# Optimization experiments

Hardware: AMD Instinct MI355X
Metric: run time of the kernel (lower is better)

Reference implementation:

```python
import jax, jax.numpy as jnp
import numpy as np

D_MODEL = 768
N_HEADS = 12
HEAD_DIM = D_MODEL // N_HEADS
D_FF = 4 * D_MODEL
EPS = 1e-5


def setup_inputs() -> dict:
    key = jax.random.key(0)
    ks = jax.random.split(key, 16)
    s = 0.02
    x = jax.random.normal(ks[0], (2, 2048, D_MODEL), dtype=jnp.float32)
    wq = jax.random.normal(ks[1], (D_MODEL, D_MODEL), dtype=jnp.float32) * s
    bq = jnp.zeros((D_MODEL,), jnp.float32)
    wk = jax.random.normal(ks[2], (D_MODEL, D_MODEL), dtype=jnp.float32) * s
    bk = jnp.zeros((D_MODEL,), jnp.float32)
    wv = jax.random.normal(ks[3], (D_MODEL, D_MODEL), dtype=jnp.float32) * s
    bv = jnp.zeros((D_MODEL,), jnp.float32)
    wo = jax.random.normal(ks[4], (D_MODEL, D_MODEL), dtype=jnp.float32) * s
    bo = jnp.zeros((D_MODEL,), jnp.float32)
    w1 = jax.random.normal(ks[5], (D_MODEL, D_FF), dtype=jnp.float32) * s
    b1 = jnp.zeros((D_FF,), jnp.float32)
    w2 = jax.random.normal(ks[6], (D_FF, D_MODEL), dtype=jnp.float32) * s
    b2 = jnp.zeros((D_MODEL,), jnp.float32)
    ln1_g = jnp.ones((D_MODEL,), jnp.float32)
    ln1_b = jnp.zeros((D_MODEL,), jnp.float32)
    ln2_g = jnp.ones((D_MODEL,), jnp.float32)
    ln2_b = jnp.zeros((D_MODEL,), jnp.float32)
    return dict(x=x, wq=wq, bq=bq, wk=wk, bk=bk, wv=wv, bv=bv, wo=wo, bo=bo,
                w1=w1, b1=b1, w2=w2, b2=b2,
                ln1_g=ln1_g, ln1_b=ln1_b, ln2_g=ln2_g, ln2_b=ln2_b)


def _layernorm(x, g, b):
    mu = jnp.mean(x, axis=-1, keepdims=True)
    var = jnp.mean(jnp.square(x - mu), axis=-1, keepdims=True)
    return (x - mu) * jax.lax.rsqrt(var + EPS) * g + b


def _attention(x, wq, bq, wk, bk, wv, bv, wo, bo):
    B, S, D = x.shape
    def split_heads(t):  # [B,S,D] -> [B,H,S,Hd]
        return t.reshape(B, S, N_HEADS, HEAD_DIM).transpose(0, 2, 1, 3)
    q = split_heads(x @ wq + bq)
    k = split_heads(x @ wk + bk)
    v = split_heads(x @ wv + bv)
    scores = jnp.einsum('bhqd,bhkd->bhqk', q, k) / np.sqrt(HEAD_DIM).astype(np.float32)
    causal = jnp.tril(jnp.ones((S, S), dtype=bool))
    scores = jnp.where(causal, scores, -jnp.inf)
    weights = jax.nn.softmax(scores, axis=-1)
    attn = jnp.einsum('bhqk,bhkd->bhqd', weights, v)
    attn = attn.transpose(0, 2, 1, 3).reshape(B, S, D)
    return attn @ wo + bo


def reference(x, wq, bq, wk, bk, wv, bv, wo, bo, w1, b1, w2, b2,
              ln1_g, ln1_b, ln2_g, ln2_b):
    x = x + _attention(_layernorm(x, ln1_g, ln1_b), wq, bq, wk, bk, wv, bv, wo, bo)
    h = _layernorm(x, ln2_g, ln2_b)
    ff = jax.nn.relu(h @ w1 + b1) @ w2 + b2
    return x + ff
```

## Files before the change

kernel.cpp:

```cpp
#include <hip/hip_runtime.h>
#include <stdint.h>

typedef __bf16 bf16;
typedef float f32x4 __attribute__((ext_vector_type(4)));
typedef bf16 bf16x8 __attribute__((ext_vector_type(8)));
typedef bf16 bf16x4 __attribute__((ext_vector_type(4)));

#define MFMA16(a, b, c) __builtin_amdgcn_mfma_f32_16x16x32_bf16((a), (b), (c), 0, 0, 0)

static __device__ __forceinline__ void load_lds16(const bf16* g, bf16* l) {
  __builtin_amdgcn_global_load_lds(
      (const __attribute__((address_space(1))) void*)g,
      (__attribute__((address_space(3))) void*)l, 16, 0, 0);
}

__global__ void __launch_bounds__(256) k_transpose(
    const float* s0, const float* s1, const float* s2, const float* s3,
    const float* s4, const float* s5,
    bf16* d0, bf16* d1, bf16* d2, bf16* d3, bf16* d4, bf16* d5) {
  int z = blockIdx.z;
  const float* src; bf16* dst; int R, C;
  switch (z) {
    case 0: src = s0; dst = d0; R = 768;  C = 768;  break;
    case 1: src = s1; dst = d1; R = 768;  C = 768;  break;
    case 2: src = s2; dst = d2; R = 768;  C = 768;  break;
    case 3: src = s3; dst = d3; R = 768;  C = 768;  break;
    case 4: src = s4; dst = d4; R = 768;  C = 3072; break;
    default: src = s5; dst = d5; R = 3072; C = 768; break;
  }
  int tcn = C >> 5;
  int nt = (R >> 5) * tcn;
  int t = blockIdx.x;
  if (t >= nt) return;
  int tr = t / tcn, tc = t % tcn;
  __shared__ float tile[32][33];
  int tx = threadIdx.x & 31, ty = threadIdx.x >> 5;
  for (int i = 0; i < 4; i++)
    tile[ty + i * 8][tx] = src[(size_t)(tr * 32 + ty + i * 8) * C + tc * 32 + tx];
  __syncthreads();
  for (int i = 0; i < 4; i++)
    dst[(size_t)(tc * 32 + ty + i * 8) * R + tr * 32 + tx] = (bf16)tile[tx][ty + i * 8];
}

__global__ void __launch_bounds__(256) k_layernorm(
    const float* __restrict__ in, const float* __restrict__ gam,
    const float* __restrict__ bet, bf16* __restrict__ out) {
  int row = blockIdx.x, tid = threadIdx.x;
  const float* rp = in + (size_t)row * 768;
  float v0 = rp[tid], v1 = rp[tid + 256], v2 = rp[tid + 512];
  float s = v0 + v1 + v2, sq = v0 * v0 + v1 * v1 + v2 * v2;
  for (int off = 1; off < 64; off <<= 1) {
    s += __shfl_xor(s, off, 64);
    sq += __shfl_xor(sq, off, 64);
  }
  __shared__ float ps[8];
  if ((tid & 63) == 0) { ps[tid >> 6] = s; ps[4 + (tid >> 6)] = sq; }
  __syncthreads();
  s = ps[0] + ps[1] + ps[2] + ps[3];
  sq = ps[4] + ps[5] + ps[6] + ps[7];
  float mu = s * (1.0f / 768.0f);
  float rstd = rsqrtf(sq * (1.0f / 768.0f) - mu * mu + 1e-5f);
  bf16* op = out + (size_t)row * 768;
  op[tid] = (bf16)((v0 - mu) * rstd * gam[tid] + bet[tid]);
  op[tid + 256] = (bf16)((v1 - mu) * rstd * gam[tid + 256] + bet[tid + 256]);
  op[tid + 512] = (bf16)((v2 - mu) * rstd * gam[tid + 512] + bet[tid + 512]);
}

__global__ void __launch_bounds__(256) k_ln2_reduce(
    const float* __restrict__ p0, const float* __restrict__ p1,
    const float* __restrict__ x, const float* __restrict__ bo,
    const float* __restrict__ gam, const float* __restrict__ bet,
    float* __restrict__ x1, bf16* __restrict__ h2) {
  int row = blockIdx.x, tid = threadIdx.x;
  size_t base = (size_t)row * 768;
  float v0 = p0[base + tid] + p1[base + tid] + x[base + tid] + bo[tid];
  float v1 = p0[base + tid + 256] + p1[base + tid + 256] + x[base + tid + 256] + bo[tid + 256];
  float v2 = p0[base + tid + 512] + p1[base + tid + 512] + x[base + tid + 512] + bo[tid + 512];
  x1[base + tid] = v0; x1[base + tid + 256] = v1; x1[base + tid + 512] = v2;
  float s = v0 + v1 + v2, sq = v0 * v0 + v1 * v1 + v2 * v2;
  for (int off = 1; off < 64; off <<= 1) {
    s += __shfl_xor(s, off, 64);
    sq += __shfl_xor(sq, off, 64);
  }
  __shared__ float ps[8];
  if ((tid & 63) == 0) { ps[tid >> 6] = s; ps[4 + (tid >> 6)] = sq; }
  __syncthreads();
  s = ps[0] + ps[1] + ps[2] + ps[3];
  sq = ps[4] + ps[5] + ps[6] + ps[7];
  float mu = s * (1.0f / 768.0f);
  float rstd = rsqrtf(sq * (1.0f / 768.0f) - mu * mu + 1e-5f);
  bf16* op = h2 + base;
  op[tid] = (bf16)((v0 - mu) * rstd * gam[tid] + bet[tid]);
  op[tid + 256] = (bf16)((v1 - mu) * rstd * gam[tid + 256] + bet[tid + 256]);
  op[tid + 512] = (bf16)((v2 - mu) * rstd * gam[tid + 512] + bet[tid + 512]);
}

__global__ void __launch_bounds__(256) k_ff2_reduce(
    const float* __restrict__ f0, const float* __restrict__ f1,
    const float* __restrict__ f2, const float* __restrict__ f3,
    const float* __restrict__ x1, const float* __restrict__ b2,
    float* __restrict__ out) {
  size_t i = ((size_t)blockIdx.x * 256 + threadIdx.x) * 4;
  int col = (int)(i % 768);
  f32x4 v = *(const f32x4*)(x1 + i);
  f32x4 b = *(const f32x4*)(b2 + col);
  f32x4 a0 = *(const f32x4*)(f0 + i), a1 = *(const f32x4*)(f1 + i);
  f32x4 a2 = *(const f32x4*)(f2 + i), a3 = *(const f32x4*)(f3 + i);
  *(f32x4*)(out + i) = v + b + a0 + a1 + a2 + a3;
}

template <int MT>
static __device__ __forceinline__ void gemm_core(
    const bf16* __restrict__ A, int lda, const bf16* __restrict__ Bt, int ldb,
    int Kc, int m0, int n0, bf16* As, bf16* Bs, f32x4 acc[MT][4]) {
  int tid = threadIdx.x, w = tid >> 6, lane = tid & 63, quad = lane >> 4, l15 = lane & 15;
  int wr = w >> 1, wc = w & 1;
  int srow = lane >> 2, sk = (lane & 3) * 8;
  for (int k0 = 0; k0 < Kc; k0 += 32) {
    __syncthreads();
    if (MT == 4) {
      for (int c = 0; c < 2; c++) {
        int seg = w * 2 + c;
        load_lds16(A + (size_t)(m0 + seg * 16 + srow) * lda + k0 + sk, As + seg * 512);
      }
    } else {
      load_lds16(A + (size_t)(m0 + w * 16 + srow) * lda + k0 + sk, As + w * 512);
    }
    for (int c = 0; c < 2; c++) {
      int seg = w * 2 + c;
      load_lds16(Bt + (size_t)(n0 + seg * 16 + srow) * ldb + k0 + sk, Bs + seg * 512);
    }
    __syncthreads();
    bf16x8 af[MT], bfr[4];
    for (int mi = 0; mi < MT; mi++)
      af[mi] = *(const bf16x8*)(As + (wr * (MT * 16) + mi * 16 + l15) * 32 + quad * 8);
    for (int ni = 0; ni < 4; ni++)
      bfr[ni] = *(const bf16x8*)(Bs + (wc * 64 + ni * 16 + l15) * 32 + quad * 8);
    for (int mi = 0; mi < MT; mi++)
      for (int ni = 0; ni < 4; ni++)
        acc[mi][ni] = MFMA16(af[mi], bfr[ni], acc[mi][ni]);
  }
}

template <int MT>
__global__ void __launch_bounds__(256) k_gemm(
    const bf16* __restrict__ A, const bf16* __restrict__ Bt,
    const float* __restrict__ bias, bf16* __restrict__ outp, int K_, int N_) {
  __shared__ __align__(16) bf16 As[MT * 32 * 32];
  __shared__ __align__(16) bf16 Bs[128 * 32];
  int m0 = blockIdx.y * (MT * 32), n0 = blockIdx.x * 128;
  f32x4 acc[MT][4] = {};
  gemm_core<MT>(A, K_, Bt, K_, K_, m0, n0, As, Bs, acc);
  int tid = threadIdx.x, w = tid >> 6, lane = tid & 63, quad = lane >> 4, l15 = lane & 15;
  int wr = w >> 1, wc = w & 1;
  float bv[4];
  for (int ni = 0; ni < 4; ni++) bv[ni] = bias[n0 + wc * 64 + ni * 16 + l15];
  for (int mi = 0; mi < MT; mi++) {
    int mb = m0 + wr * (MT * 16) + mi * 16 + quad * 4;
    for (int ni = 0; ni < 4; ni++) {
      int n = n0 + wc * 64 + ni * 16 + l15;
      for (int r = 0; r < 4; r++) {
        float val = acc[mi][ni][r] + bv[ni];
        outp[(size_t)(mb + r) * N_ + n] = (bf16)fmaxf(val, 0.0f);
      }
    }
  }
}

template <int MT>
__global__ void __launch_bounds__(256) k_gemm_split(
    const bf16* __restrict__ A, const bf16* __restrict__ Bt,
    float* __restrict__ f0, float* __restrict__ f1,
    float* __restrict__ f2, float* __restrict__ f3, int K_, int Kc, int N_) {
  __shared__ __align__(16) bf16 As[MT * 32 * 32];
  __shared__ __align__(16) bf16 Bs[128 * 32];
  int z = blockIdx.z;
  float* outp = (z == 0) ? f0 : (z == 1) ? f1 : (z == 2) ? f2 : f3;
  int m0 = blockIdx.y * (MT * 32), n0 = blockIdx.x * 128;
  f32x4 acc[MT][4] = {};
  gemm_core<MT>(A + (size_t)z * Kc, K_, Bt + (size_t)z * Kc, K_, Kc, m0, n0, As, Bs, acc);
  int tid = threadIdx.x, w = tid >> 6, lane = tid & 63, quad = lane >> 4, l15 = lane & 15;
  int wr = w >> 1, wc = w & 1;
  for (int mi = 0; mi < MT; mi++) {
    int mb = m0 + wr * (MT * 16) + mi * 16 + quad * 4;
    for (int ni = 0; ni < 4; ni++) {
      int n = n0 + wc * 64 + ni * 16 + l15;
      for (int r = 0; r < 4; r++)
        outp[(size_t)(mb + r) * N_ + n] = acc[mi][ni][r];
    }
  }
}

template <int MT>
__global__ void __launch_bounds__(256) k_gemm_qkv(
    const bf16* __restrict__ h1, const bf16* __restrict__ wqT,
    const bf16* __restrict__ wkT, const bf16* __restrict__ wvT,
    const float* __restrict__ bq, const float* __restrict__ bk,
    const float* __restrict__ bv, bf16* __restrict__ qb,
    bf16* __restrict__ kb, bf16* __restrict__ vtb) {
  __shared__ __align__(16) bf16 As[MT * 32 * 32];
  __shared__ __align__(16) bf16 Bs[128 * 32];
  int z = blockIdx.z;
  const bf16* Bt = (z == 0) ? wqT : (z == 1) ? wkT : wvT;
  const float* bias = (z == 0) ? bq : (z == 1) ? bk : bv;
  int m0 = blockIdx.y * (MT * 32), n0 = blockIdx.x * 128;
  f32x4 acc[MT][4] = {};
  gemm_core<MT>(h1, 768, Bt, 768, 768, m0, n0, As, Bs, acc);
  int tid = threadIdx.x, w = tid >> 6, lane = tid & 63, quad = lane >> 4, l15 = lane & 15;
  int wr = w >> 1, wc = w & 1;
  float bvv[4];
  for (int ni = 0; ni < 4; ni++) bvv[ni] = bias[n0 + wc * 64 + ni * 16 + l15];
  for (int mi = 0; mi < MT; mi++) {
    int mb = m0 + wr * (MT * 16) + mi * 16 + quad * 4;
    int b = mb >> 11, s0_ = mb & 2047;
    for (int ni = 0; ni < 4; ni++) {
      int n = n0 + wc * 64 + ni * 16 + l15;
      int h = n >> 6, hd = n & 63;
      if (z < 2) {
        bf16* outp = (z == 0) ? qb : kb;
        size_t base = (size_t)(b * 12 + h) * 2048 * 64;
        for (int r = 0; r < 4; r++)
          outp[base + (size_t)(s0_ + r) * 64 + hd] = (bf16)(acc[mi][ni][r] + bvv[ni]);
      } else {
        bf16x4 pk;
        for (int r = 0; r < 4; r++) pk[r] = (bf16)(acc[mi][ni][r] + bvv[ni]);
        *(bf16x4*)(vtb + (((size_t)(b * 12 + h) * 64 + hd) * 2048 + s0_)) = pk;
      }
    }
  }
}

__global__ void __launch_bounds__(256) k_attn(
    const bf16* __restrict__ qb, const bf16* __restrict__ kb,
    const bf16* __restrict__ vtb, bf16* __restrict__ out) {
  __shared__ __align__(16) bf16 Ks[128 * 64];
  __shared__ __align__(16) bf16 Vs[64 * 128];
  __shared__ __align__(16) bf16 Ps[4][16 * 128];
  int qt = 31 - (blockIdx.x / 24);
  int bh = blockIdx.x % 24;
  int q0 = qt * 64;
  int tid = threadIdx.x, w = tid >> 6, lane = tid & 63, quad = lane >> 4, l15 = lane & 15;
  const bf16* qbase = qb + (size_t)bh * 2048 * 64;
  const bf16* kbase = kb + (size_t)bh * 2048 * 64;
  const bf16* vbase = vtb + (size_t)bh * 64 * 2048;

  bf16x8 qf[2];
  for (int ds = 0; ds < 2; ds++)
    qf[ds] = *(const bf16x8*)(qbase + (size_t)(q0 + w * 16 + l15) * 64 + ds * 32 + quad * 8);

  f32x4 o[4] = {};
  f32x4 l_i = {};

  const float C2 = 0.18033688011112042f;
  int nkt = (qt >> 1) + 1;
  for (int kt = 0; kt < nkt; kt++) {
    int k0 = kt * 128;
    __syncthreads();
    {
      int rsub = lane >> 3, c8 = lane & 7;
      for (int c = 0; c < 4; c++) {
        int seg = c * 4 + w;
        int row = seg * 8 + rsub;
        load_lds16(kbase + (size_t)(k0 + row) * 64 + ((c8 ^ (row & 7)) * 8), Ks + seg * 512);
      }
      int rsub2 = lane >> 4, c16 = lane & 15;
      for (int c = 0; c < 4; c++) {
        int seg = c * 4 + w;
        int row = seg * 4 + rsub2;
        load_lds16(vbase + (size_t)row * 2048 + k0 + ((c16 ^ (row & 15)) * 8), Vs + seg * 512);
      }
    }
    __syncthreads();

    f32x4 sc[8] = {};
    for (int kj = 0; kj < 8; kj++) {
      int krow = kj * 16 + l15;
      for (int ds = 0; ds < 2; ds++) {
        bf16x8 kf = *(const bf16x8*)(Ks + krow * 64 + (((ds * 4 + quad) ^ (krow & 7)) * 8));
        sc[kj] = MFMA16(qf[ds], kf, sc[kj]);
      }
    }
    if (kt == nkt - 1) {
      int qg = q0 + w * 16 + quad * 4;
      for (int kj = 0; kj < 8; kj++) {
        int kg = k0 + kj * 16 + l15;
        for (int r = 0; r < 4; r++)
          if (kg > qg + r) sc[kj][r] = -3.0e38f;
      }
    }
    f32x4 lsum = {};
    for (int kj = 0; kj < 8; kj++)
      for (int r = 0; r < 4; r++) {
        float p = exp2f(sc[kj][r] * C2);
        sc[kj][r] = p;
        lsum[r] += p;
      }
    for (int off = 1; off < 16; off <<= 1)
      for (int r = 0; r < 4; r++) lsum[r] += __shfl_xor(lsum[r], off, 64);
    for (int r = 0; r < 4; r++) l_i[r] += lsum[r];
    for (int kj = 0; kj < 8; kj++) {
      int colb = kj * 16 + l15;
      int chb = colb >> 3, cin = colb & 7;
      for (int r = 0; r < 4; r++) {
        int prow = quad * 4 + r;
        Ps[w][prow * 128 + ((chb ^ prow) * 8) + cin] = (bf16)sc[kj][r];
      }
    }
    for (int ks = 0; ks < 4; ks++) {
      int prow = l15;
      bf16x8 pf = *(const bf16x8*)(&Ps[w][prow * 128 + (((ks * 4 + quad) ^ prow) * 8)]);
      for (int dj = 0; dj < 4; dj++) {
        int vrow = dj * 16 + l15;
        bf16x8 vf = *(const bf16x8*)(Vs + vrow * 128 + (((ks * 4 + quad) ^ (vrow & 15)) * 8));
        o[dj] = MFMA16(pf, vf, o[dj]);
      }
    }
  }
  int b = bh / 12, h = bh % 12;
  f32x4 rl;
  for (int r = 0; r < 4; r++) rl[r] = 1.0f / l_i[r];
  int srow = q0 + w * 16 + quad * 4;
  for (int dj = 0; dj < 4; dj++) {
    int d = h * 64 + dj * 16 + l15;
    for (int r = 0; r < 4; r++)
      out[(size_t)(b * 2048 + srow + r) * 768 + d] = (bf16)(o[dj][r] * rl[r]);
  }
}

extern "C" void kernel_launch(void* const* d_in, const int* in_sizes, int n_in,
                              void* d_out, int out_size, void* d_ws, size_t ws_size,
                              hipStream_t stream) {
  const float* x    = (const float*)d_in[0];
  const float* wq   = (const float*)d_in[1];
  const float* bq   = (const float*)d_in[2];
  const float* wk   = (const float*)d_in[3];
  const float* bk   = (const float*)d_in[4];
  const float* wv   = (const float*)d_in[5];
  const float* bv   = (const float*)d_in[6];
  const float* wo   = (const float*)d_in[7];
  const float* bo   = (const float*)d_in[8];
  const float* w1   = (const float*)d_in[9];
  const float* b1   = (const float*)d_in[10];
  const float* w2   = (const float*)d_in[11];
  const float* b2   = (const float*)d_in[12];
  const float* ln1g = (const float*)d_in[13];
  const float* ln1b = (const float*)d_in[14];
  const float* ln2g = (const float*)d_in[15];
  const float* ln2b = (const float*)d_in[16];

  char* p = (char*)d_ws;
  bf16* wqT = (bf16*)p; p += (size_t)768 * 768 * 2;
  bf16* wkT = (bf16*)p; p += (size_t)768 * 768 * 2;
  bf16* wvT = (bf16*)p; p += (size_t)768 * 768 * 2;
  bf16* woT = (bf16*)p; p += (size_t)768 * 768 * 2;
  bf16* w1T = (bf16*)p; p += (size_t)768 * 3072 * 2;
  bf16* w2T = (bf16*)p; p += (size_t)768 * 3072 * 2;
  bf16* h1   = (bf16*)p; p += (size_t)4096 * 768 * 2;
  bf16* qbuf = (bf16*)p; p += (size_t)4096 * 768 * 2;
  bf16* kbuf = (bf16*)p; p += (size_t)4096 * 768 * 2;
  bf16* vtb  = (bf16*)p; p += (size_t)4096 * 768 * 2;
  bf16* att  = (bf16*)p; p += (size_t)4096 * 768 * 2;
  float* x1  = (float*)p; p += (size_t)4096 * 768 * 4;
  bf16* h2   = (bf16*)p; p += (size_t)4096 * 768 * 2;
  bf16* ffm  = (bf16*)p; p += (size_t)4096 * 3072 * 2;
  float* p0  = (float*)p; p += (size_t)4096 * 768 * 4;
  float* p1  = (float*)p; p += (size_t)4096 * 768 * 4;
  float* f0 = (float*)h1;
  float* f1 = (float*)kbuf;
  float* f2 = p0;
  float* f3 = p1;

  k_transpose<<<dim3(2304, 1, 6), dim3(256), 0, stream>>>(
      wq, wk, wv, wo, w1, w2, wqT, wkT, wvT, woT, w1T, w2T);
  k_layernorm<<<dim3(4096), dim3(256), 0, stream>>>(x, ln1g, ln1b, h1);
  k_gemm_qkv<2><<<dim3(6, 64, 3), dim3(256), 0, stream>>>(
      h1, wqT, wkT, wvT, bq, bk, bv, qbuf, kbuf, vtb);
  k_attn<<<dim3(768), dim3(256), 0, stream>>>(qbuf, kbuf, vtb, att);
  k_gemm_split<2><<<dim3(6, 64, 2), dim3(256), 0, stream>>>(
      att, woT, p0, p1, p0, p1, 768, 384, 768);
  k_ln2_reduce<<<dim3(4096), dim3(256), 0, stream>>>(
      p0, p1, x, bo, ln2g, ln2b, x1, h2);
  k_gemm<2><<<dim3(24, 64), dim3(256), 0, stream>>>(
      h2, w1T, b1, ffm, 768, 3072);
  k_gemm_split<2><<<dim3(6, 64, 4), dim3(256), 0, stream>>>(
      ffm, w2T, f0, f1, f2, f3, 3072, 768, 768);
  k_ff2_reduce<<<dim3(3072), dim3(256), 0, stream>>>(
      f0, f1, f2, f3, x1, b2, (float*)d_out);
}
```

Baseline: 315.7 us.

## Double-buffer GEMM and attention K tiles, read V from global, enlarge FFN tiles

GEMM cores now keep two LDS buffers and issue the next K-slice's global-to-LDS loads before computing on the current one. This drops one barrier per iteration and lets loads overlap MFMA work. Attention double-buffers only the K tile and reads V fragments straight from global memory instead of staging them in LDS. The two FFN GEMMs switch to the larger MT=4 tiles, and all these kernels get an occupancy hint of 3 blocks per CU. The trade-offs are more LDS per block, strided uncached-in-LDS V reads that rely on L2, and fewer blocks for the FFN GEMMs.

```diff
diff --git a/kernel.cpp b/kernel.cpp
--- a/kernel.cpp
+++ b/kernel.cpp
@@ -116,38 +116,51 @@
   int tid = threadIdx.x, w = tid >> 6, lane = tid & 63, quad = lane >> 4, l15 = lane & 15;
   int wr = w >> 1, wc = w & 1;
   int srow = lane >> 2, sk = (lane & 3) * 8;
-  for (int k0 = 0; k0 < Kc; k0 += 32) {
-    __syncthreads();
+  const int ABUF = MT * 32 * 32;
+  const int BBUF = 128 * 32;
+
+  auto stage = [&](int k0, int buf) {
+    bf16* Ab = As + buf * ABUF;
+    bf16* Bb = Bs + buf * BBUF;
     if (MT == 4) {
       for (int c = 0; c < 2; c++) {
         int seg = w * 2 + c;
-        load_lds16(A + (size_t)(m0 + seg * 16 + srow) * lda + k0 + sk, As + seg * 512);
+        load_lds16(A + (size_t)(m0 + seg * 16 + srow) * lda + k0 + sk, Ab + seg * 512);
       }
     } else {
-      load_lds16(A + (size_t)(m0 + w * 16 + srow) * lda + k0 + sk, As + w * 512);
+      load_lds16(A + (size_t)(m0 + w * 16 + srow) * lda + k0 + sk, Ab + w * 512);
     }
     for (int c = 0; c < 2; c++) {
       int seg = w * 2 + c;
-      load_lds16(Bt + (size_t)(n0 + seg * 16 + srow) * ldb + k0 + sk, Bs + seg * 512);
-    }
+      load_lds16(Bt + (size_t)(n0 + seg * 16 + srow) * ldb + k0 + sk, Bb + seg * 512);
+    }
+  };
+
+  stage(0, 0);
+  int cur = 0;
+  for (int k0 = 0; k0 < Kc; k0 += 32) {
     __syncthreads();
+    if (k0 + 32 < Kc) stage(k0 + 32, cur ^ 1);
+    const bf16* Ab = As + cur * ABUF;
+    const bf16* Bb = Bs + cur * BBUF;
     bf16x8 af[MT], bfr[4];
     for (int mi = 0; mi < MT; mi++)
-      af[mi] = *(const bf16x8*)(As + (wr * (MT * 16) + mi * 16 + l15) * 32 + quad * 8);
+      af[mi] = *(const bf16x8*)(Ab + (wr * (MT * 16) + mi * 16 + l15) * 32 + quad * 8);
     for (int ni = 0; ni < 4; ni++)
-      bfr[ni] = *(const bf16x8*)(Bs + (wc * 64 + ni * 16 + l15) * 32 + quad * 8);
+      bfr[ni] = *(const bf16x8*)(Bb + (wc * 64 + ni * 16 + l15) * 32 + quad * 8);
     for (int mi = 0; mi < MT; mi++)
       for (int ni = 0; ni < 4; ni++)
         acc[mi][ni] = MFMA16(af[mi], bfr[ni], acc[mi][ni]);
+    cur ^= 1;
   }
 }
 
 template <int MT>
-__global__ void __launch_bounds__(256) k_gemm(
+__global__ void __launch_bounds__(256, 3) k_gemm(
     const bf16* __restrict__ A, const bf16* __restrict__ Bt,
     const float* __restrict__ bias, bf16* __restrict__ outp, int K_, int N_) {
-  __shared__ __align__(16) bf16 As[MT * 32 * 32];
-  __shared__ __align__(16) bf16 Bs[128 * 32];
+  __shared__ __align__(16) bf16 As[2 * MT * 32 * 32];
+  __shared__ __align__(16) bf16 Bs[2 * 128 * 32];
   int m0 = blockIdx.y * (MT * 32), n0 = blockIdx.x * 128;
   f32x4 acc[MT][4] = {};
   gemm_core<MT>(A, K_, Bt, K_, K_, m0, n0, As, Bs, acc);
@@ -168,12 +181,12 @@
 }
 
 template <int MT>
-__global__ void __launch_bounds__(256) k_gemm_split(
+__global__ void __launch_bounds__(256, 3) k_gemm_split(
     const bf16* __restrict__ A, const bf16* __restrict__ Bt,
     float* __restrict__ f0, float* __restrict__ f1,
     float* __restrict__ f2, float* __restrict__ f3, int K_, int Kc, int N_) {
-  __shared__ __align__(16) bf16 As[MT * 32 * 32];
-  __shared__ __align__(16) bf16 Bs[128 * 32];
+  __shared__ __align__(16) bf16 As[2 * MT * 32 * 32];
+  __shared__ __align__(16) bf16 Bs[2 * 128 * 32];
   int z = blockIdx.z;
   float* outp = (z == 0) ? f0 : (z == 1) ? f1 : (z == 2) ? f2 : f3;
   int m0 = blockIdx.y * (MT * 32), n0 = blockIdx.x * 128;
@@ -192,14 +205,14 @@
 }
 
 template <int MT>
-__global__ void __launch_bounds__(256) k_gemm_qkv(
+__global__ void __launch_bounds__(256, 3) k_gemm_qkv(
     const bf16* __restrict__ h1, const bf16* __restrict__ wqT,
     const bf16* __restrict__ wkT, const bf16* __restrict__ wvT,
     const float* __restrict__ bq, const float* __restrict__ bk,
     const float* __restrict__ bv, bf16* __restrict__ qb,
     bf16* __restrict__ kb, bf16* __restrict__ vtb) {
-  __shared__ __align__(16) bf16 As[MT * 32 * 32];
-  __shared__ __align__(16) bf16 Bs[128 * 32];
+  __shared__ __align__(16) bf16 As[2 * MT * 32 * 32];
+  __shared__ __align__(16) bf16 Bs[2 * 128 * 32];
   int z = blockIdx.z;
   const bf16* Bt = (z == 0) ? wqT : (z == 1) ? wkT : wvT;
   const float* bias = (z == 0) ? bq : (z == 1) ? bk : bv;
@@ -230,11 +243,10 @@
   }
 }
 
-__global__ void __launch_bounds__(256) k_attn(
+__global__ void __launch_bounds__(256, 3) k_attn(
     const bf16* __restrict__ qb, const bf16* __restrict__ kb,
     const bf16* __restrict__ vtb, bf16* __restrict__ out) {
-  __shared__ __align__(16) bf16 Ks[128 * 64];
-  __shared__ __align__(16) bf16 Vs[64 * 128];
+  __shared__ __align__(16) bf16 Ks[2 * 128 * 64];
   __shared__ __align__(16) bf16 Ps[4][16 * 128];
   int qt = 31 - (blockIdx.x / 24);
   int bh = blockIdx.x % 24;
@@ -251,32 +263,31 @@
   f32x4 o[4] = {};
   f32x4 l_i = {};
 
+  auto stageK = [&](int k0, int buf) {
+    int rsub = lane >> 3, c8 = lane & 7;
+    bf16* Kb = Ks + buf * (128 * 64);
+    for (int c = 0; c < 4; c++) {
+      int seg = c * 4 + w;
+      int row = seg * 8 + rsub;
+      load_lds16(kbase + (size_t)(k0 + row) * 64 + ((c8 ^ (row & 7)) * 8), Kb + seg * 512);
+    }
+  };
+
   const float C2 = 0.18033688011112042f;
   int nkt = (qt >> 1) + 1;
+  stageK(0, 0);
+  int cur = 0;
   for (int kt = 0; kt < nkt; kt++) {
     int k0 = kt * 128;
     __syncthreads();
-    {
-      int rsub = lane >> 3, c8 = lane & 7;
-      for (int c = 0; c < 4; c++) {
-        int seg = c * 4 + w;
-        int row = seg * 8 + rsub;
-        load_lds16(kbase + (size_t)(k0 + row) * 64 + ((c8 ^ (row & 7)) * 8), Ks + seg * 512);
-      }
-      int rsub2 = lane >> 4, c16 = lane & 15;
-      for (int c = 0; c < 4; c++) {
-        int seg = c * 4 + w;
-        int row = seg * 4 + rsub2;
-        load_lds16(vbase + (size_t)row * 2048 + k0 + ((c16 ^ (row & 15)) * 8), Vs + seg * 512);
-      }
-    }
-    __syncthreads();
+    if (kt + 1 < nkt) stageK(k0 + 128, cur ^ 1);
+    const bf16* Kb = Ks + cur * (128 * 64);
 
     f32x4 sc[8] = {};
     for (int kj = 0; kj < 8; kj++) {
       int krow = kj * 16 + l15;
       for (int ds = 0; ds < 2; ds++) {
-        bf16x8 kf = *(const bf16x8*)(Ks + krow * 64 + (((ds * 4 + quad) ^ (krow & 7)) * 8));
+        bf16x8 kf = *(const bf16x8*)(Kb + krow * 64 + (((ds * 4 + quad) ^ (krow & 7)) * 8));
         sc[kj] = MFMA16(qf[ds], kf, sc[kj]);
       }
     }
@@ -311,10 +322,11 @@
       bf16x8 pf = *(const bf16x8*)(&Ps[w][prow * 128 + (((ks * 4 + quad) ^ prow) * 8)]);
       for (int dj = 0; dj < 4; dj++) {
         int vrow = dj * 16 + l15;
-        bf16x8 vf = *(const bf16x8*)(Vs + vrow * 128 + (((ks * 4 + quad) ^ (vrow & 15)) * 8));
+        bf16x8 vf = *(const bf16x8*)(vbase + (size_t)vrow * 2048 + k0 + (ks * 4 + quad) * 8);
         o[dj] = MFMA16(pf, vf, o[dj]);
       }
     }
+    cur ^= 1;
   }
   int b = bh / 12, h = bh % 12;
   f32x4 rl;
@@ -380,9 +392,9 @@
       att, woT, p0, p1, p0, p1, 768, 384, 768);
   k_ln2_reduce<<<dim3(4096), dim3(256), 0, stream>>>(
       p0, p1, x, bo, ln2g, ln2b, x1, h2);
-  k_gemm<2><<<dim3(24, 64), dim3(256), 0, stream>>>(
+  k_gemm<4><<<dim3(24, 32), dim3(256), 0, stream>>>(
       h2, w1T, b1, ffm, 768, 3072);
-  k_gemm_split<2><<<dim3(6, 64, 4), dim3(256), 0, stream>>>(
+  k_gemm_split<4><<<dim3(6, 32, 4), dim3(256), 0, stream>>>(
       ffm, w2T, f0, f1, f2, f3, 3072, 768, 768);
   k_ff2_reduce<<<dim3(3072), dim3(256), 0, stream>>>(
       f0, f1, f2, f3, x1, b2, (float*)d_out);
```

Measured after the change: 328.3 us. +4.0%, slower.
